# Optimization experiments

Measured on AMD Instinct MI355X. Metric: run time of the kernel, lower is better.

The kernel has to match this reference:

```python
import jax, jax.numpy as jnp
import numpy as np

B, S, D_MODEL = 2, 2048, 2048
N_HEADS, N_KV_HEADS, HEAD_DIM = 32, 8, 64
N_GROUPS = N_HEADS // N_KV_HEADS


def setup_inputs() -> dict:
    key = jax.random.key(0)
    ks = jax.random.split(key, 5)
    x = jax.random.normal(ks[0], (B, S, D_MODEL), dtype=jnp.float32)
    wq = jax.random.normal(ks[1], (N_HEADS * HEAD_DIM, D_MODEL), dtype=jnp.float32) * 0.02
    wk = jax.random.normal(ks[2], (N_KV_HEADS * HEAD_DIM, D_MODEL), dtype=jnp.float32) * 0.02
    wv = jax.random.normal(ks[3], (N_KV_HEADS * HEAD_DIM, D_MODEL), dtype=jnp.float32) * 0.02
    wo = jax.random.normal(ks[4], (D_MODEL, N_HEADS * HEAD_DIM), dtype=jnp.float32) * 0.02
    # Rotary tables: module's apply_rope expects cos/sin of shape [S, head_dim//2]
    half = HEAD_DIM // 2
    inv_freq = 1.0 / (10000.0 ** (jnp.arange(0, half, dtype=jnp.float32) / half))
    angles = jnp.arange(S, dtype=jnp.float32)[:, None] * inv_freq[None, :]  # [S, half]
    cos = jnp.cos(angles)
    sin = jnp.sin(angles)
    return {"x": x, "wq": wq, "wk": wk, "wv": wv, "wo": wo, "cos": cos, "sin": sin}


def _rotate_half(t):
    half = t.shape[-1] // 2
    return jnp.concatenate((-t[..., half:], t[..., :half]), axis=-1)


def _apply_rope(q, k, cos, sin):
    # cos/sin: [S, head_dim//2] -> repeat_interleave(2) -> [S, head_dim]
    cos2 = jnp.repeat(cos, 2, axis=-1)[None, :, None, :]  # [1,S,1,D]
    sin2 = jnp.repeat(sin, 2, axis=-1)[None, :, None, :]
    q_rot = q * cos2 + _rotate_half(q) * sin2
    k_rot = k * cos2 + _rotate_half(k) * sin2
    return q_rot, k_rot


def reference(x, wq, wk, wv, wo, cos, sin):
    b, s, _ = x.shape
    q = (x @ wq.T).reshape(b, s, N_HEADS, HEAD_DIM)
    k = (x @ wk.T).reshape(b, s, N_KV_HEADS, HEAD_DIM)
    v = (x @ wv.T).reshape(b, s, N_KV_HEADS, HEAD_DIM)
    q, k = _apply_rope(q, k, cos, sin)
    # GQA expansion: repeat_interleave along head dim
    k = jnp.repeat(k, N_GROUPS, axis=2)  # [b,s,H,D]
    v = jnp.repeat(v, N_GROUPS, axis=2)
    q = q.transpose(0, 2, 1, 3)  # [b,H,s,D]
    k = k.transpose(0, 2, 1, 3)
    v = v.transpose(0, 2, 1, 3)
    scale = HEAD_DIM ** -0.5
    scores = jnp.einsum("bhqd,bhkd->bhqk", q, k) * scale
    causal = jnp.tril(jnp.ones((s, s), dtype=bool))
    scores = jnp.where(causal[None, None], scores, jnp.finfo(scores.dtype).min)
    attn = jax.nn.softmax(scores, axis=-1)
    out = jnp.einsum("bhqk,bhkd->bhqd", attn, v)
    out = out.transpose(0, 2, 1, 3).reshape(b, s, N_HEADS * HEAD_DIM)
    return out @ wo.T
```

## Files before the change

### kernel.cpp

```cpp
#include <hip/hip_runtime.h>
#include <hip/hip_bf16.h>

#define B_   2
#define S_   2048
#define DM   2048
#define NH   32
#define NKV  8
#define HD   64
#define MROWS 4096
#define NQKV  3072

typedef __attribute__((ext_vector_type(8))) short bf16x8;
typedef __attribute__((ext_vector_type(4))) float f32x4;
typedef __attribute__((ext_vector_type(16))) float f32x16;

__device__ __forceinline__ unsigned short f2b(float f) {
  __hip_bfloat16 h = __float2bfloat16(f);
  return *reinterpret_cast<unsigned short*>(&h);
}

__device__ __forceinline__ void gload16(const void* g, void* l) {
  __builtin_amdgcn_global_load_lds((__attribute__((address_space(1))) void*)g,
                                   (__attribute__((address_space(3))) void*)l,
                                   16, 0, 0);
}

__device__ __forceinline__ unsigned cvtpk(float lo, float hi) {
  unsigned r;
  asm("v_cvt_pk_bf16_f32 %0, %1, %2" : "=v"(r) : "v"(lo), "v"(hi));
  return r;
}

__device__ __forceinline__ void pl32swap(unsigned& a, unsigned& b) {
  asm volatile("v_permlane32_swap_b32 %0, %1" : "+v"(a), "+v"(b));
}

__device__ __forceinline__ float exp2hw(float x) {
  float r;
  asm("v_exp_f32 %0, %1" : "=v"(r) : "v"(x));
  return r;
}

__device__ __forceinline__ bf16x8 mk8(unsigned w0, unsigned w1, unsigned w2, unsigned w3) {
  union { unsigned u[4]; bf16x8 v; } uu;
  uu.u[0] = w0; uu.u[1] = w1; uu.u[2] = w2; uu.u[3] = w3;
  return uu.v;
}

__global__ __launch_bounds__(256) void f2bf_kernel(const float* __restrict__ in,
                                                   unsigned short* __restrict__ out, int n4) {
  int i = blockIdx.x * 256 + threadIdx.x;
  if (i < n4) {
    float4 v = reinterpret_cast<const float4*>(in)[i];
    ushort4 o;
    o.x = f2b(v.x); o.y = f2b(v.y); o.z = f2b(v.z); o.w = f2b(v.w);
    reinterpret_cast<ushort4*>(out)[i] = o;
  }
}

__global__ __launch_bounds__(256) void wcat_kernel(const float* __restrict__ wq,
                                                   const float* __restrict__ wk,
                                                   const float* __restrict__ wv,
                                                   unsigned short* __restrict__ out) {
  int i = blockIdx.x * 256 + threadIdx.x;
  int e = i * 4;
  int row = e >> 11;
  int col = e & 2047;
  const float* src;
  if (row < 2048)      src = wq + (size_t)row * 2048 + col;
  else if (row < 2560) src = wk + (size_t)(row - 2048) * 2048 + col;
  else                 src = wv + (size_t)(row - 2560) * 2048 + col;
  float4 v = *reinterpret_cast<const float4*>(src);
  ushort4 o;
  o.x = f2b(v.x); o.y = f2b(v.y); o.z = f2b(v.z); o.w = f2b(v.w);
  reinterpret_cast<ushort4*>(out)[i] = o;
}

#define BMg 256
#define BNg 128
#define BKg 64
__global__ __launch_bounds__(512, 2) void gemm_bt(const unsigned short* __restrict__ A,
                                                  const unsigned short* __restrict__ Bm,
                                                  float* __restrict__ C,
                                                  int M, int N, int K) {
  __shared__ unsigned short Abuf[3][BMg * BKg];
  __shared__ unsigned short Bbuf[3][BNg * BKg];
  const int tid = threadIdx.x;
  const int wave = tid >> 6, lane = tid & 63;
  const int wr = wave >> 1, wc = wave & 1;
  const int rowbase = blockIdx.y * BMg;
  const int colbase = blockIdx.x * BNg;
  const unsigned short* Ag = A + (size_t)rowbase * K;
  const unsigned short* Bg = Bm + (size_t)colbase * K;
  const int NT = K / BKg;

  auto stage_half = [&](int buf, int k0, int half) {
#pragma unroll
    for (int i = 0; i < 2; ++i) {
      int c = wave * 256 + (half * 2 + i) * 64 + lane;
      int r = c >> 3, p = c & 7;
      gload16(Ag + (size_t)r * K + k0 + ((p ^ (r & 7)) << 3),
              &Abuf[buf][(wave * 256 + (half * 2 + i) * 64) * 8]);
    }
    int c = wave * 128 + half * 64 + lane;
    int r = c >> 3, p = c & 7;
    gload16(Bg + (size_t)r * K + k0 + ((p ^ (r & 7)) << 3),
            &Bbuf[buf][(wave * 128 + half * 64) * 8]);
  };
  auto ldA = [&](int buf, int row, int c16) -> bf16x8 {
    return *(const bf16x8*)((const char*)&Abuf[buf][0] + row * 128 + ((c16 ^ (row & 7)) << 4));
  };
  auto ldB = [&](int buf, int row, int c16) -> bf16x8 {
    return *(const bf16x8*)((const char*)&Bbuf[buf][0] + row * 128 + ((c16 ^ (row & 7)) << 4));
  };

  f32x4 acc[4][4];
#pragma unroll
  for (int a = 0; a < 4; a++)
#pragma unroll
    for (int b2 = 0; b2 < 4; b2++) acc[a][b2] = (f32x4){0.f, 0.f, 0.f, 0.f};

  const int l15 = lane & 15, l4 = lane >> 4;

  stage_half(0, 0, 0); stage_half(0, 0, 1);
  stage_half(1, BKg, 0); stage_half(1, BKg, 1);
  asm volatile("s_waitcnt vmcnt(6)" ::: "memory");
  __builtin_amdgcn_s_barrier();

  int cur = 0;
  for (int t = 0; t < NT; ++t) {
    const int nxt2 = (cur >= 1) ? cur - 1 : cur + 2;
    {
      bf16x8 af[4], bfv[4];
#pragma unroll
      for (int mt = 0; mt < 4; ++mt) af[mt] = ldA(cur, wr * 64 + mt * 16 + l15, l4);
#pragma unroll
      for (int nt = 0; nt < 4; ++nt) bfv[nt] = ldB(cur, wc * 64 + nt * 16 + l15, l4);
      if (t + 2 < NT) stage_half(nxt2, (t + 2) * BKg, 0);
      __builtin_amdgcn_s_barrier();
      __builtin_amdgcn_s_setprio(1);
#pragma unroll
      for (int mt = 0; mt < 4; ++mt)
#pragma unroll
        for (int nt = 0; nt < 4; ++nt)
          acc[mt][nt] = __builtin_amdgcn_mfma_f32_16x16x32_bf16(af[mt], bfv[nt], acc[mt][nt], 0, 0, 0);
      __builtin_amdgcn_s_setprio(0);
      __builtin_amdgcn_s_barrier();
    }
    {
      bf16x8 af[4], bfv[4];
#pragma unroll
      for (int mt = 0; mt < 4; ++mt) af[mt] = ldA(cur, wr * 64 + mt * 16 + l15, 4 + l4);
#pragma unroll
      for (int nt = 0; nt < 4; ++nt) bfv[nt] = ldB(cur, wc * 64 + nt * 16 + l15, 4 + l4);
      if (t + 2 < NT) stage_half(nxt2, (t + 2) * BKg, 1);
      __builtin_amdgcn_s_barrier();
      __builtin_amdgcn_s_setprio(1);
#pragma unroll
      for (int mt = 0; mt < 4; ++mt)
#pragma unroll
        for (int nt = 0; nt < 4; ++nt)
          acc[mt][nt] = __builtin_amdgcn_mfma_f32_16x16x32_bf16(af[mt], bfv[nt], acc[mt][nt], 0, 0, 0);
      __builtin_amdgcn_s_setprio(0);
      if (t < NT - 1) {
        if (t + 2 < NT) asm volatile("s_waitcnt vmcnt(6)" ::: "memory");
        else            asm volatile("s_waitcnt vmcnt(0)" ::: "memory");
        __builtin_amdgcn_s_barrier();
      }
    }
    cur = (cur < 2) ? cur + 1 : 0;
  }

  const int orow = rowbase + wr * 64, ocol = colbase + wc * 64;
#pragma unroll
  for (int mt = 0; mt < 4; mt++)
#pragma unroll
    for (int nt = 0; nt < 4; nt++)
#pragma unroll
      for (int r = 0; r < 4; r++)
        C[(size_t)(orow + mt * 16 + l4 * 4 + r) * N + ocol + nt * 16 + l15] = acc[mt][nt][r];
}

#define QSCALE 0.18033688011112042f
__global__ __launch_bounds__(256) void rope_kernel(const float* __restrict__ qkv,
                                                   const float* __restrict__ cosg,
                                                   const float* __restrict__ sing,
                                                   unsigned short* __restrict__ Qb,
                                                   unsigned short* __restrict__ Kb,
                                                   unsigned short* __restrict__ Vtb) {
  const int row = blockIdx.x;
  const int b = row >> 11, s = row & 2047;
  __shared__ float cs[32], sn[32];
  if (threadIdx.x < 32) {
    cs[threadIdx.x] = cosg[s * 32 + threadIdx.x];
    sn[threadIdx.x] = sing[s * 32 + threadIdx.x];
  }
  __syncthreads();
  const float* qr = qkv + (size_t)row * NQKV;
  const int t = threadIdx.x;

  for (int pid = t; pid < 1024; pid += 256) {
    const int h = pid >> 5, i = pid & 31, i2 = i >> 1;
    float qa = qr[h * 64 + i], qb2 = qr[h * 64 + i + 32];
    size_t base = ((size_t)(b * NH + h) * S_ + s) * HD;
    Qb[base + i]      = f2b((qa * cs[i2] - qb2 * sn[i2]) * QSCALE);
    Qb[base + i + 32] = f2b((qb2 * cs[16 + i2] + qa * sn[16 + i2]) * QSCALE);
  }
  {
    const int h = t >> 5, i = t & 31, i2 = i >> 1;
    float ka = qr[2048 + h * 64 + i], kb2 = qr[2048 + h * 64 + i + 32];
    size_t base = ((size_t)(b * NKV + h) * S_ + s) * HD;
    Kb[base + i]      = f2b(ka * cs[i2] - kb2 * sn[i2]);
    Kb[base + i + 32] = f2b(kb2 * cs[16 + i2] + ka * sn[16 + i2]);
  }
  for (int j = t; j < 512; j += 256) {
    const int h = j >> 6, d = j & 63;
    Vtb[((size_t)(b * NKV + h) * HD + d) * S_ + s] = f2b(qr[2560 + j]);
  }
}

__device__ __forceinline__ void stage_kv(const unsigned short* __restrict__ Kbase,
                                         const unsigned short* __restrict__ Vbase,
                                         unsigned short* Kl, unsigned short* Vl,
                                         int j0, int wave, int lane) {
#pragma unroll
  for (int tt = 0; tt < 2; ++tt) {
    int slot = (wave * 2 + tt) * 64 + lane;
    int row = slot >> 3, blk = slot & 7;
    int sb = ((blk ^ (row & 7)) << 3);
    gload16(Kbase + (size_t)(j0 + row) * HD + sb, Kl + (wave * 2 + tt) * 512);
    gload16(Vbase + (size_t)row * S_ + j0 + sb, Vl + (wave * 2 + tt) * 512);
  }
}

__global__ __launch_bounds__(256) void attn_kernel(const unsigned short* __restrict__ Q,
                                                   const unsigned short* __restrict__ Kg,
                                                   const unsigned short* __restrict__ Vt,
                                                   unsigned short* __restrict__ AO) {
  const int pr = blockIdx.x, h = blockIdx.y, b = blockIdx.z;
  const int hk = h >> 2;
  __shared__ unsigned short kv_lds[16384];
  __shared__ unsigned short ow_lds[9216];
  const int tid = threadIdx.x, wave = tid >> 6, lane = tid & 63;
  const int l31 = lane & 31, hi = lane >> 5;

  const unsigned short* Qbase = Q + (size_t)(b * NH + h) * S_ * HD;
  const unsigned short* Kbase = Kg + (size_t)(b * NKV + hk) * S_ * HD;
  const unsigned short* Vbase = Vt + (size_t)(b * NKV + hk) * HD * S_;

  const int NT_B = 2 * (16 - pr);
  const int NTtot = 34;

  stage_kv(Kbase, Vbase, kv_lds, kv_lds + 8192, 0, wave, lane);
  __syncthreads();
  int cur = 0;
  int tlin = 0;

  for (int rg = 0; rg < 2; ++rg) {
    const int qbi = rg == 0 ? (15 - pr) : pr;
    const int qb = qbi * 128;
    const int NT = 2 * (qbi + 1);
    const int q0w = qb + wave * 32;
    const int qg = q0w + l31;

    bf16x8 qf[4];
#pragma unroll
    for (int c = 0; c < 4; ++c)
      qf[c] = *reinterpret_cast<const bf16x8*>(Qbase + (size_t)qg * HD + c * 16 + hi * 8);

    f32x16 Oa0 = {}, Oa1 = {};
    float m_old = -INFINITY, lsum = 0.f;

    for (int t = 0; t < NT; ++t, ++tlin) {
      const int j0 = t * 64;
      const int tn = tlin + 1;
      if (tn < NTtot) {
        const int j0n = (tn < NT_B ? tn : tn - NT_B) * 64;
        stage_kv(Kbase, Vbase, kv_lds + (cur ^ 1) * 4096, kv_lds + 8192 + (cur ^ 1) * 4096,
                 j0n, wave, lane);
      }

      if (j0 < q0w + 32) {
        const char* Klc = (const char*)(kv_lds + cur * 4096);
        const char* Vlc = (const char*)(kv_lds + 8192 + cur * 4096);

        f32x16 s0 = {}, s1 = {};
        __builtin_amdgcn_s_setprio(1);
#pragma unroll
        for (int c = 0; c < 4; ++c) {
          const int r0 = l31;
          bf16x8 kf = *(const bf16x8*)(Klc + r0 * 128 + ((((c << 1) + hi) ^ (r0 & 7)) << 4));
          s0 = __builtin_amdgcn_mfma_f32_32x32x16_bf16(kf, qf[c], s0, 0, 0, 0);
        }
#pragma unroll
        for (int c = 0; c < 4; ++c) {
          const int r1 = 32 + l31;
          bf16x8 kf = *(const bf16x8*)(Klc + r1 * 128 + ((((c << 1) + hi) ^ (r1 & 7)) << 4));
          s1 = __builtin_amdgcn_mfma_f32_32x32x16_bf16(kf, qf[c], s1, 0, 0, 0);
        }
        __builtin_amdgcn_s_setprio(0);

        const bool need_mask = (j0 + 63 > q0w);
        const int kb0 = j0 + 4 * hi, kb1 = j0 + 32 + 4 * hi;
        if (need_mask) {
#pragma unroll
          for (int r = 0; r < 16; ++r) {
            const int ko = (r & 3) + 8 * (r >> 2);
            if (kb0 + ko > qg) s0[r] = -INFINITY;
            if (kb1 + ko > qg) s1[r] = -INFINITY;
          }
        }

        float a0 = fmaxf(s0[0], s1[0]), a1 = fmaxf(s0[1], s1[1]);
        float a2 = fmaxf(s0[2], s1[2]), a3 = fmaxf(s0[3], s1[3]);
#pragma unroll
        for (int r = 4; r < 16; r += 4) {
          a0 = fmaxf(a0, fmaxf(s0[r], s1[r]));
          a1 = fmaxf(a1, fmaxf(s0[r + 1], s1[r + 1]));
          a2 = fmaxf(a2, fmaxf(s0[r + 2], s1[r + 2]));
          a3 = fmaxf(a3, fmaxf(s0[r + 3], s1[r + 3]));
        }
        float mxt = fmaxf(fmaxf(a0, a1), fmaxf(a2, a3));
        mxt = fmaxf(mxt, __shfl_xor(mxt, 32, 64));

        if (!__all(mxt - m_old <= 8.f)) {
          float mnew = fmaxf(m_old, mxt);
          float corr = exp2hw(m_old - mnew);
          m_old = mnew;
          lsum *= corr;
#pragma unroll
          for (int r = 0; r < 16; ++r) { Oa0[r] *= corr; Oa1[r] *= corr; }
        }

        float t0 = 0.f, t1 = 0.f, t2 = 0.f, t3 = 0.f;
#pragma unroll
        for (int r = 0; r < 16; r += 4) {
          s0[r]     = exp2hw(s0[r] - m_old);     t0 += s0[r];
          s0[r + 1] = exp2hw(s0[r + 1] - m_old); t1 += s0[r + 1];
          s0[r + 2] = exp2hw(s0[r + 2] - m_old); t2 += s0[r + 2];
          s0[r + 3] = exp2hw(s0[r + 3] - m_old); t3 += s0[r + 3];
        }
#pragma unroll
        for (int r = 0; r < 16; r += 4) {
          s1[r]     = exp2hw(s1[r] - m_old);     t0 += s1[r];
          s1[r + 1] = exp2hw(s1[r + 1] - m_old); t1 += s1[r + 1];
          s1[r + 2] = exp2hw(s1[r + 2] - m_old); t2 += s1[r + 2];
          s1[r + 3] = exp2hw(s1[r + 3] - m_old); t3 += s1[r + 3];
        }
        float rs = (t0 + t1) + (t2 + t3);
        rs += __shfl_xor(rs, 32, 64);
        lsum += rs;

        unsigned a0u = cvtpk(s0[0], s0[1]),  b0u = cvtpk(s0[4], s0[5]);  pl32swap(a0u, b0u);
        unsigned a1u = cvtpk(s0[2], s0[3]),  b1u = cvtpk(s0[6], s0[7]);  pl32swap(a1u, b1u);
        bf16x8 pf00 = mk8(a0u, a1u, b0u, b1u);
        unsigned a2u = cvtpk(s0[8], s0[9]),  b2u = cvtpk(s0[12], s0[13]); pl32swap(a2u, b2u);
        unsigned a3u = cvtpk(s0[10], s0[11]), b3u = cvtpk(s0[14], s0[15]); pl32swap(a3u, b3u);
        bf16x8 pf01 = mk8(a2u, a3u, b2u, b3u);
        unsigned a4u = cvtpk(s1[0], s1[1]),  b4u = cvtpk(s1[4], s1[5]);  pl32swap(a4u, b4u);
        unsigned a5u = cvtpk(s1[2], s1[3]),  b5u = cvtpk(s1[6], s1[7]);  pl32swap(a5u, b5u);
        bf16x8 pf10 = mk8(a4u, a5u, b4u, b5u);
        unsigned a6u = cvtpk(s1[8], s1[9]),  b6u = cvtpk(s1[12], s1[13]); pl32swap(a6u, b6u);
        unsigned a7u = cvtpk(s1[10], s1[11]), b7u = cvtpk(s1[14], s1[15]); pl32swap(a7u, b7u);
        bf16x8 pf11 = mk8(a6u, a7u, b6u, b7u);

        __builtin_amdgcn_s_setprio(1);
#pragma unroll
        for (int sk = 0; sk < 4; ++sk) {
          const int s = sk >> 1, kc = sk & 1;
          const bf16x8 pf = (sk == 0) ? pf00 : (sk == 1) ? pf01 : (sk == 2) ? pf10 : pf11;
          {
            const int row = l31;
            bf16x8 vf = *(const bf16x8*)(Vlc + row * 128 +
                          ((((s << 2) + (kc << 1) + hi) ^ (row & 7)) << 4));
            Oa0 = __builtin_amdgcn_mfma_f32_32x32x16_bf16(vf, pf, Oa0, 0, 0, 0);
          }
          {
            const int row = 32 + l31;
            bf16x8 vf = *(const bf16x8*)(Vlc + row * 128 +
                          ((((s << 2) + (kc << 1) + hi) ^ (row & 7)) << 4));
            Oa1 = __builtin_amdgcn_mfma_f32_32x32x16_bf16(vf, pf, Oa1, 0, 0, 0);
          }
        }
        __builtin_amdgcn_s_setprio(0);
      }
      __syncthreads();
      cur ^= 1;
    }

    unsigned short* ow = ow_lds + wave * 2304;
    const float inv = 1.0f / lsum;
#pragma unroll
    for (int r = 0; r < 16; ++r) {
      const int dl = (r & 3) + 8 * (r >> 2) + 4 * hi;
      ow[l31 * 72 + dl]      = f2b(Oa0[r] * inv);
      ow[l31 * 72 + 32 + dl] = f2b(Oa1[r] * inv);
    }
    __syncthreads();
#pragma unroll
    for (int it = 0; it < 4; ++it) {
      const int idx = it * 64 + lane;
      const int row = idx >> 3, blkk = idx & 7;
      bf16x8 v = *(const bf16x8*)(ow + row * 72 + blkk * 8);
      *(bf16x8*)(AO + (size_t)(b * S_ + qb + wave * 32 + row) * 2048 + h * 64 + blkk * 8) = v;
    }
  }
}

extern "C" void kernel_launch(void* const* d_in, const int* in_sizes, int n_in,
                              void* d_out, int out_size, void* d_ws, size_t ws_size,
                              hipStream_t stream) {
  (void)in_sizes; (void)n_in; (void)out_size; (void)ws_size;
  const float* x    = (const float*)d_in[0];
  const float* wq   = (const float*)d_in[1];
  const float* wk   = (const float*)d_in[2];
  const float* wv   = (const float*)d_in[3];
  const float* wo   = (const float*)d_in[4];
  const float* cosg = (const float*)d_in[5];
  const float* sing = (const float*)d_in[6];

  char* ws = (char*)d_ws;
  unsigned short* xb   = (unsigned short*)(ws);
  unsigned short* wcat = (unsigned short*)(ws + 16777216);
  unsigned short* wob  = (unsigned short*)(ws + 29360128);
  float*          qkv  = (float*)         (ws + 37748736);
  unsigned short* Qb   = (unsigned short*)(ws + 88080384);
  unsigned short* Kb   = (unsigned short*)(ws + 104857600);
  unsigned short* Vtb  = (unsigned short*)(ws + 109051904);
  unsigned short* AO   = xb;

  f2bf_kernel<<<8192, 256, 0, stream>>>(x, xb, 2097152);
  wcat_kernel<<<6144, 256, 0, stream>>>(wq, wk, wv, wcat);
  f2bf_kernel<<<4096, 256, 0, stream>>>(wo, wob, 1048576);

  gemm_bt<<<dim3(NQKV / BNg, MROWS / BMg), 512, 0, stream>>>(xb, wcat, qkv, MROWS, NQKV, DM);

  rope_kernel<<<MROWS, 256, 0, stream>>>(qkv, cosg, sing, Qb, Kb, Vtb);

  attn_kernel<<<dim3(8, NH, B_), 256, 0, stream>>>(Qb, Kb, Vtb, AO);

  gemm_bt<<<dim3(DM / BNg, MROWS / BMg), 512, 0, stream>>>(AO, wob, (float*)d_out, MROWS, DM, DM);
}
```

Measured before the change: 226.7 us.

## Fuse RoPE and QKV layout into GEMM epilogue; triple-buffer attention K/V

Adds a QKV GEMM variant whose epilogue applies RoPE and the Q scale, then writes bf16 Q and K in token-major layout and V transposed. This removes the fp32 qkv intermediate and the separate rope kernel. Attention now reads Q and K with a row stride and uses a 3-deep K/V LDS ring with vmcnt waits in place of double buffering and a full __syncthreads each step. Its output goes straight to global memory without LDS staging. The trade-off is scattered 2-byte epilogue stores, strided Q/K reads and more LDS per attention block.

```diff
diff --git a/kernel.cpp b/kernel.cpp
--- a/kernel.cpp
+++ b/kernel.cpp
@@ -79,6 +79,161 @@
 #define BMg 256
 #define BNg 128
 #define BKg 64
+#define QSCALE 0.18033688011112042f
+
+__global__ __launch_bounds__(512, 2) void gemm_qkv(const unsigned short* __restrict__ A,
+                                                   const unsigned short* __restrict__ Bm,
+                                                   unsigned short* __restrict__ Qb,
+                                                   unsigned short* __restrict__ Kb2,
+                                                   unsigned short* __restrict__ Vtb,
+                                                   const float* __restrict__ cosg,
+                                                   const float* __restrict__ sing) {
+  const int K = DM;
+  __shared__ unsigned short Abuf[3][BMg * BKg];
+  __shared__ unsigned short Bbuf[3][BNg * BKg];
+  const int tid = threadIdx.x;
+  const int wave = tid >> 6, lane = tid & 63;
+  const int wr = wave >> 1, wc = wave & 1;
+  const int rowbase = blockIdx.y * BMg;
+  const int colbase = blockIdx.x * BNg;
+  const unsigned short* Ag = A + (size_t)rowbase * K;
+  const unsigned short* Bg = Bm + (size_t)colbase * K;
+  const int NT = K / BKg;
+
+  auto stage_half = [&](int buf, int k0, int half) {
+#pragma unroll
+    for (int i = 0; i < 2; ++i) {
+      int c = wave * 256 + (half * 2 + i) * 64 + lane;
+      int r = c >> 3, p = c & 7;
+      gload16(Ag + (size_t)r * K + k0 + ((p ^ (r & 7)) << 3),
+              &Abuf[buf][(wave * 256 + (half * 2 + i) * 64) * 8]);
+    }
+    int c = wave * 128 + half * 64 + lane;
+    int r = c >> 3, p = c & 7;
+    gload16(Bg + (size_t)r * K + k0 + ((p ^ (r & 7)) << 3),
+            &Bbuf[buf][(wave * 128 + half * 64) * 8]);
+  };
+  auto ldA = [&](int buf, int row, int c16) -> bf16x8 {
+    return *(const bf16x8*)((const char*)&Abuf[buf][0] + row * 128 + ((c16 ^ (row & 7)) << 4));
+  };
+  auto ldB = [&](int buf, int row, int c16) -> bf16x8 {
+    return *(const bf16x8*)((const char*)&Bbuf[buf][0] + row * 128 + ((c16 ^ (row & 7)) << 4));
+  };
+
+  f32x4 acc[4][4];
+#pragma unroll
+  for (int a = 0; a < 4; a++)
+#pragma unroll
+    for (int b2 = 0; b2 < 4; b2++) acc[a][b2] = (f32x4){0.f, 0.f, 0.f, 0.f};
+
+  const int l15 = lane & 15, l4 = lane >> 4;
+
+  stage_half(0, 0, 0); stage_half(0, 0, 1);
+  stage_half(1, BKg, 0); stage_half(1, BKg, 1);
+  asm volatile("s_waitcnt vmcnt(6)" ::: "memory");
+  __builtin_amdgcn_s_barrier();
+
+  int cur = 0;
+  for (int t = 0; t < NT; ++t) {
+    const int nxt2 = (cur >= 1) ? cur - 1 : cur + 2;
+    {
+      bf16x8 af[4], bfv[4];
+#pragma unroll
+      for (int mt = 0; mt < 4; ++mt) af[mt] = ldA(cur, wr * 64 + mt * 16 + l15, l4);
+#pragma unroll
+      for (int nt = 0; nt < 4; ++nt) bfv[nt] = ldB(cur, wc * 64 + nt * 16 + l15, l4);
+      if (t + 2 < NT) stage_half(nxt2, (t + 2) * BKg, 0);
+      __builtin_amdgcn_s_barrier();
+      __builtin_amdgcn_s_setprio(1);
+#pragma unroll
+      for (int mt = 0; mt < 4; ++mt)
+#pragma unroll
+        for (int nt = 0; nt < 4; ++nt)
+          acc[mt][nt] = __builtin_amdgcn_mfma_f32_16x16x32_bf16(af[mt], bfv[nt], acc[mt][nt], 0, 0, 0);
+      __builtin_amdgcn_s_setprio(0);
+      __builtin_amdgcn_s_barrier();
+    }
+    {
+      bf16x8 af[4], bfv[4];
+#pragma unroll
+      for (int mt = 0; mt < 4; ++mt) af[mt] = ldA(cur, wr * 64 + mt * 16 + l15, 4 + l4);
+#pragma unroll
+      for (int nt = 0; nt < 4; ++nt) bfv[nt] = ldB(cur, wc * 64 + nt * 16 + l15, 4 + l4);
+      if (t + 2 < NT) stage_half(nxt2, (t + 2) * BKg, 1);
+      __builtin_amdgcn_s_barrier();
+      __builtin_amdgcn_s_setprio(1);
+#pragma unroll
+      for (int mt = 0; mt < 4; ++mt)
+#pragma unroll
+        for (int nt = 0; nt < 4; ++nt)
+          acc[mt][nt] = __builtin_amdgcn_mfma_f32_16x16x32_bf16(af[mt], bfv[nt], acc[mt][nt], 0, 0, 0);
+      __builtin_amdgcn_s_setprio(0);
+      if (t < NT - 1) {
+        if (t + 2 < NT) asm volatile("s_waitcnt vmcnt(6)" ::: "memory");
+        else            asm volatile("s_waitcnt vmcnt(0)" ::: "memory");
+        __builtin_amdgcn_s_barrier();
+      }
+    }
+    cur = (cur < 2) ? cur + 1 : 0;
+  }
+
+  const int orow = rowbase + wr * 64, ocol = colbase + wc * 64;
+  if (colbase < 2048) {
+#pragma unroll
+    for (int mt = 0; mt < 4; ++mt)
+#pragma unroll
+      for (int r = 0; r < 4; ++r) {
+        const int row = orow + mt * 16 + l4 * 4 + r;
+        const int s = row & 2047;
+        const float* cR = cosg + s * 32;
+        const float* sR = sing + s * 32;
+#pragma unroll
+        for (int nt = 0; nt < 2; ++nt) {
+          const int i2 = nt * 8 + (l15 >> 1);
+          float c0 = cR[i2], sv0 = sR[i2], c1 = cR[16 + i2], sv1 = sR[16 + i2];
+          float alo = acc[mt][nt][r], ahi = acc[mt][nt + 2][r];
+          size_t base = (size_t)row * 2048 + ocol + nt * 16 + l15;
+          Qb[base]      = f2b((alo * c0 - ahi * sv0) * QSCALE);
+          Qb[base + 32] = f2b((ahi * c1 + alo * sv1) * QSCALE);
+        }
+      }
+  } else if (colbase < 2560) {
+    const int kcol = ocol - 2048;
+#pragma unroll
+    for (int mt = 0; mt < 4; ++mt)
+#pragma unroll
+      for (int r = 0; r < 4; ++r) {
+        const int row = orow + mt * 16 + l4 * 4 + r;
+        const int s = row & 2047;
+        const float* cR = cosg + s * 32;
+        const float* sR = sing + s * 32;
+#pragma unroll
+        for (int nt = 0; nt < 2; ++nt) {
+          const int i2 = nt * 8 + (l15 >> 1);
+          float c0 = cR[i2], sv0 = sR[i2], c1 = cR[16 + i2], sv1 = sR[16 + i2];
+          float alo = acc[mt][nt][r], ahi = acc[mt][nt + 2][r];
+          size_t base = (size_t)row * 512 + kcol + nt * 16 + l15;
+          Kb2[base]      = f2b(alo * c0 - ahi * sv0);
+          Kb2[base + 32] = f2b(ahi * c1 + alo * sv1);
+        }
+      }
+  } else {
+    const int hkv = (ocol - 2560) >> 6;
+#pragma unroll
+    for (int mt = 0; mt < 4; ++mt)
+#pragma unroll
+      for (int nt = 0; nt < 4; ++nt) {
+        const int d = nt * 16 + l15;
+        const int row0 = orow + mt * 16 + l4 * 4;
+        const int b = row0 >> 11, s0i = row0 & 2047;
+        ushort4 u;
+        u.x = f2b(acc[mt][nt][0]); u.y = f2b(acc[mt][nt][1]);
+        u.z = f2b(acc[mt][nt][2]); u.w = f2b(acc[mt][nt][3]);
+        *(ushort4*)(Vtb + ((size_t)(b * NKV + hkv) * HD + d) * S_ + s0i) = u;
+      }
+  }
+}
+
 __global__ __launch_bounds__(512, 2) void gemm_bt(const unsigned short* __restrict__ A,
                                                   const unsigned short* __restrict__ Bm,
                                                   float* __restrict__ C,
@@ -181,80 +336,42 @@
         C[(size_t)(orow + mt * 16 + l4 * 4 + r) * N + ocol + nt * 16 + l15] = acc[mt][nt][r];
 }
 
-#define QSCALE 0.18033688011112042f
-__global__ __launch_bounds__(256) void rope_kernel(const float* __restrict__ qkv,
-                                                   const float* __restrict__ cosg,
-                                                   const float* __restrict__ sing,
-                                                   unsigned short* __restrict__ Qb,
-                                                   unsigned short* __restrict__ Kb,
-                                                   unsigned short* __restrict__ Vtb) {
-  const int row = blockIdx.x;
-  const int b = row >> 11, s = row & 2047;
-  __shared__ float cs[32], sn[32];
-  if (threadIdx.x < 32) {
-    cs[threadIdx.x] = cosg[s * 32 + threadIdx.x];
-    sn[threadIdx.x] = sing[s * 32 + threadIdx.x];
-  }
-  __syncthreads();
-  const float* qr = qkv + (size_t)row * NQKV;
-  const int t = threadIdx.x;
-
-  for (int pid = t; pid < 1024; pid += 256) {
-    const int h = pid >> 5, i = pid & 31, i2 = i >> 1;
-    float qa = qr[h * 64 + i], qb2 = qr[h * 64 + i + 32];
-    size_t base = ((size_t)(b * NH + h) * S_ + s) * HD;
-    Qb[base + i]      = f2b((qa * cs[i2] - qb2 * sn[i2]) * QSCALE);
-    Qb[base + i + 32] = f2b((qb2 * cs[16 + i2] + qa * sn[16 + i2]) * QSCALE);
-  }
-  {
-    const int h = t >> 5, i = t & 31, i2 = i >> 1;
-    float ka = qr[2048 + h * 64 + i], kb2 = qr[2048 + h * 64 + i + 32];
-    size_t base = ((size_t)(b * NKV + h) * S_ + s) * HD;
-    Kb[base + i]      = f2b(ka * cs[i2] - kb2 * sn[i2]);
-    Kb[base + i + 32] = f2b(kb2 * cs[16 + i2] + ka * sn[16 + i2]);
-  }
-  for (int j = t; j < 512; j += 256) {
-    const int h = j >> 6, d = j & 63;
-    Vtb[((size_t)(b * NKV + h) * HD + d) * S_ + s] = f2b(qr[2560 + j]);
-  }
-}
-
-__device__ __forceinline__ void stage_kv(const unsigned short* __restrict__ Kbase,
-                                         const unsigned short* __restrict__ Vbase,
-                                         unsigned short* Kl, unsigned short* Vl,
-                                         int j0, int wave, int lane) {
-#pragma unroll
-  for (int tt = 0; tt < 2; ++tt) {
-    int slot = (wave * 2 + tt) * 64 + lane;
-    int row = slot >> 3, blk = slot & 7;
-    int sb = ((blk ^ (row & 7)) << 3);
-    gload16(Kbase + (size_t)(j0 + row) * HD + sb, Kl + (wave * 2 + tt) * 512);
-    gload16(Vbase + (size_t)row * S_ + j0 + sb, Vl + (wave * 2 + tt) * 512);
-  }
-}
-
-__global__ __launch_bounds__(256) void attn_kernel(const unsigned short* __restrict__ Q,
-                                                   const unsigned short* __restrict__ Kg,
+__global__ __launch_bounds__(256) void attn_kernel(const unsigned short* __restrict__ Qb,
+                                                   const unsigned short* __restrict__ Kb2,
                                                    const unsigned short* __restrict__ Vt,
                                                    unsigned short* __restrict__ AO) {
   const int pr = blockIdx.x, h = blockIdx.y, b = blockIdx.z;
   const int hk = h >> 2;
-  __shared__ unsigned short kv_lds[16384];
-  __shared__ unsigned short ow_lds[9216];
+  __shared__ unsigned short Kbuf[3][4096];
+  __shared__ unsigned short Vbuf[3][4096];
   const int tid = threadIdx.x, wave = tid >> 6, lane = tid & 63;
   const int l31 = lane & 31, hi = lane >> 5;
 
-  const unsigned short* Qbase = Q + (size_t)(b * NH + h) * S_ * HD;
-  const unsigned short* Kbase = Kg + (size_t)(b * NKV + hk) * S_ * HD;
+  const unsigned short* Qrow = Qb + (size_t)b * S_ * 2048 + h * 64;
+  const unsigned short* Krow = Kb2 + (size_t)b * S_ * 512 + hk * 64;
   const unsigned short* Vbase = Vt + (size_t)(b * NKV + hk) * HD * S_;
 
   const int NT_B = 2 * (16 - pr);
   const int NTtot = 34;
 
-  stage_kv(Kbase, Vbase, kv_lds, kv_lds + 8192, 0, wave, lane);
-  __syncthreads();
-  int cur = 0;
-  int tlin = 0;
+  auto j0_of = [&](int tl) { return (tl < NT_B ? tl : tl - NT_B) * 64; };
+  auto stage = [&](int j0, int bufi) {
+#pragma unroll
+    for (int tt = 0; tt < 2; ++tt) {
+      int slot = (wave * 2 + tt) * 64 + lane;
+      int row = slot >> 3, blk = slot & 7;
+      int sb = ((blk ^ (row & 7)) << 3);
+      gload16(Krow + (size_t)(j0 + row) * 512 + sb, &Kbuf[bufi][(wave * 2 + tt) * 512]);
+      gload16(Vbase + (size_t)row * S_ + j0 + sb, &Vbuf[bufi][(wave * 2 + tt) * 512]);
+    }
+  };
+
+  stage(0, 0);
+  stage(j0_of(1), 1);
+  asm volatile("s_waitcnt vmcnt(4)" ::: "memory");
+  __builtin_amdgcn_s_barrier();
+
+  int cur = 0, tlin = 0;
 
   for (int rg = 0; rg < 2; ++rg) {
     const int qbi = rg == 0 ? (15 - pr) : pr;
@@ -266,23 +383,18 @@
     bf16x8 qf[4];
 #pragma unroll
     for (int c = 0; c < 4; ++c)
-      qf[c] = *reinterpret_cast<const bf16x8*>(Qbase + (size_t)qg * HD + c * 16 + hi * 8);
+      qf[c] = *reinterpret_cast<const bf16x8*>(Qrow + (size_t)qg * 2048 + c * 16 + hi * 8);
 
     f32x16 Oa0 = {}, Oa1 = {};
     float m_old = -INFINITY, lsum = 0.f;
 
     for (int t = 0; t < NT; ++t, ++tlin) {
       const int j0 = t * 64;
-      const int tn = tlin + 1;
-      if (tn < NTtot) {
-        const int j0n = (tn < NT_B ? tn : tn - NT_B) * 64;
-        stage_kv(Kbase, Vbase, kv_lds + (cur ^ 1) * 4096, kv_lds + 8192 + (cur ^ 1) * 4096,
-                 j0n, wave, lane);
-      }
+      if (tlin + 2 < NTtot) stage(j0_of(tlin + 2), cur >= 1 ? cur - 1 : cur + 2);
 
       if (j0 < q0w + 32) {
-        const char* Klc = (const char*)(kv_lds + cur * 4096);
-        const char* Vlc = (const char*)(kv_lds + 8192 + cur * 4096);
+        const char* Klc = (const char*)&Kbuf[cur][0];
+        const char* Vlc = (const char*)&Vbuf[cur][0];
 
         f32x16 s0 = {}, s1 = {};
         __builtin_amdgcn_s_setprio(1);
@@ -384,25 +496,26 @@
         }
         __builtin_amdgcn_s_setprio(0);
       }
-      __syncthreads();
-      cur ^= 1;
-    }
-
-    unsigned short* ow = ow_lds + wave * 2304;
+
+      if (tlin + 1 < NTtot) {
+        if (tlin + 2 < NTtot) asm volatile("s_waitcnt vmcnt(4)" ::: "memory");
+        else                  asm volatile("s_waitcnt vmcnt(0)" ::: "memory");
+        __builtin_amdgcn_s_barrier();
+      }
+      cur = (cur < 2) ? cur + 1 : 0;
+    }
+
     const float inv = 1.0f / lsum;
-#pragma unroll
-    for (int r = 0; r < 16; ++r) {
-      const int dl = (r & 3) + 8 * (r >> 2) + 4 * hi;
-      ow[l31 * 72 + dl]      = f2b(Oa0[r] * inv);
-      ow[l31 * 72 + 32 + dl] = f2b(Oa1[r] * inv);
-    }
-    __syncthreads();
-#pragma unroll
-    for (int it = 0; it < 4; ++it) {
-      const int idx = it * 64 + lane;
-      const int row = idx >> 3, blkk = idx & 7;
-      bf16x8 v = *(const bf16x8*)(ow + row * 72 + blkk * 8);
-      *(bf16x8*)(AO + (size_t)(b * S_ + qb + wave * 32 + row) * 2048 + h * 64 + blkk * 8) = v;
+    unsigned short* ob = AO + (size_t)(b * S_ + qg) * 2048 + h * 64;
+#pragma unroll
+    for (int c = 0; c < 4; ++c) {
+      ushort4 u0, u1;
+      u0.x = f2b(Oa0[4 * c] * inv);     u0.y = f2b(Oa0[4 * c + 1] * inv);
+      u0.z = f2b(Oa0[4 * c + 2] * inv); u0.w = f2b(Oa0[4 * c + 3] * inv);
+      u1.x = f2b(Oa1[4 * c] * inv);     u1.y = f2b(Oa1[4 * c + 1] * inv);
+      u1.z = f2b(Oa1[4 * c + 2] * inv); u1.w = f2b(Oa1[4 * c + 3] * inv);
+      *(ushort4*)(ob + 8 * c + 4 * hi)      = u0;
+      *(ushort4*)(ob + 32 + 8 * c + 4 * hi) = u1;
     }
   }
 }
@@ -416,28 +529,27 @@
   const float* wk   = (const float*)d_in[2];
   const float* wv   = (const float*)d_in[3];
   const float* wo   = (const float*)d_in[4];
+  const float* wo_  = wo;
   const float* cosg = (const float*)d_in[5];
   const float* sing = (const float*)d_in[6];
+  (void)wo_;
 
   char* ws = (char*)d_ws;
   unsigned short* xb   = (unsigned short*)(ws);
   unsigned short* wcat = (unsigned short*)(ws + 16777216);
   unsigned short* wob  = (unsigned short*)(ws + 29360128);
-  float*          qkv  = (float*)         (ws + 37748736);
-  unsigned short* Qb   = (unsigned short*)(ws + 88080384);
-  unsigned short* Kb   = (unsigned short*)(ws + 104857600);
-  unsigned short* Vtb  = (unsigned short*)(ws + 109051904);
+  unsigned short* Qb   = (unsigned short*)(ws + 37748736);
+  unsigned short* Kb2  = (unsigned short*)(ws + 54525952);
+  unsigned short* Vtb  = (unsigned short*)(ws + 58720256);
   unsigned short* AO   = xb;
 
   f2bf_kernel<<<8192, 256, 0, stream>>>(x, xb, 2097152);
   wcat_kernel<<<6144, 256, 0, stream>>>(wq, wk, wv, wcat);
   f2bf_kernel<<<4096, 256, 0, stream>>>(wo, wob, 1048576);
 
-  gemm_bt<<<dim3(NQKV / BNg, MROWS / BMg), 512, 0, stream>>>(xb, wcat, qkv, MROWS, NQKV, DM);
-
-  rope_kernel<<<MROWS, 256, 0, stream>>>(qkv, cosg, sing, Qb, Kb, Vtb);
-
-  attn_kernel<<<dim3(8, NH, B_), 256, 0, stream>>>(Qb, Kb, Vtb, AO);
+  gemm_qkv<<<dim3(NQKV / BNg, MROWS / BMg), 512, 0, stream>>>(xb, wcat, Qb, Kb2, Vtb, cosg, sing);
+
+  attn_kernel<<<dim3(8, NH, B_), 256, 0, stream>>>(Qb, Kb2, Vtb, AO);
 
   gemm_bt<<<dim3(DM / BNg, MROWS / BMg), 512, 0, stream>>>(AO, wob, (float*)d_out, MROWS, DM, DM);
 }
```

Result: faster. 203.6 us (-10.2%).
